# Performance work log

Hardware: AMD Instinct MI355X
Metric: run time of the kernel (lower is better)

## Reference

```python
import jax, jax.numpy as jnp
import numpy as np

K_WEIGHT = 1.7  # K passed in original forward: w(t, H, 1.7)
B_EXP = 2.5     # default exponent b in w()


def setup_inputs() -> dict:
    key = jax.random.key(0)
    k1, k2 = jax.random.split(key)
    B, H, D = 512, 2048, 64
    pred = jax.random.normal(k1, (B, H, D), dtype=jnp.float32)
    targ = jax.random.normal(k2, (B, H, D), dtype=jnp.float32)
    return {"pred": pred, "targ": targ}


def reference(pred, targ):
    # pred, targ: [B, H, D]
    B, H, D = pred.shape
    # t_i = number of nonzero entries of targ[i, :, 1] along horizon
    t = jnp.sum((targ[:, :, 1] != 0).astype(pred.dtype), axis=1)  # [B]
    # w(t, T=H, K=1.7, b=2.5) = 1 + (K-1) * (t/(H-1))**b
    weight = 1.0 + (K_WEIGHT - 1.0) * (t / (H - 1)) ** B_EXP      # [B]
    idx = t.astype(jnp.int32) - 1                                  # [B], scatter row per sample
    # Only channel 0 of the squared error is ever used (loss[:, :, :1]);
    # the [B,H,1]*[B,H,D] broadcast + sum over D is equivalent to *D.
    loss0 = (pred[:, :, 0] - targ[:, :, 0]) ** 2                   # [B, H]
    gathered = jnp.take_along_axis(loss0, idx[:, None], axis=1)[:, 0]  # [B]
    weighted_loss = jnp.mean(gathered * weight * D)
    return weighted_loss
```

## Files before the change

### kernel.cpp

```cpp
#include <hip/hip_runtime.h>


#define BB 512
#define HH 2048
#define DD 64

__global__ __launch_bounds__(256) void WeightedStateLoss4_kernel(
    const float* __restrict__ pred,
    const float* __restrict__ targ,
    float* __restrict__ out)
{
    const int i   = blockIdx.x;
    const int tid = threadIdx.x;

    const float* trow = targ + (size_t)i * HH * DD;

    int cnt = 0;
    float v[HH / 256];
#pragma unroll
    for (int k = 0; k < HH / 256; ++k) {
        const int h = tid + k * 256;
        v[k] = trow[(size_t)h * DD + 1];
    }
#pragma unroll
    for (int k = 0; k < HH / 256; ++k) {
        cnt += (v[k] != 0.0f) ? 1 : 0;
    }

#pragma unroll
    for (int off = 32; off > 0; off >>= 1)
        cnt += __shfl_down(cnt, off, 64);

    __shared__ int s[4];
    const int wave = tid >> 6;
    const int lane = tid & 63;
    if (lane == 0) s[wave] = cnt;
    __syncthreads();

    if (tid == 0) {
        const int t = s[0] + s[1] + s[2] + s[3];
        const float tf = (float)t;
        const float ratio = tf / (float)(HH - 1);
        const float w = 1.0f + 0.7f * powf(ratio, 2.5f);

        int idx = t - 1;
        idx = idx < 0 ? 0 : (idx > HH - 1 ? HH - 1 : idx);

        const size_t base = ((size_t)i * HH + (size_t)idx) * DD;
        const float p = pred[base];
        const float q = targ[base];
        const float d = p - q;
        const float val = d * d * w * (float)DD * (1.0f / (float)BB);
        atomicAdd(out, val);
    }
}

extern "C" void kernel_launch(void* const* d_in, const int* in_sizes, int n_in,
                              void* d_out, int out_size, void* d_ws, size_t ws_size,
                              hipStream_t stream)
{
    const float* pred = (const float*)d_in[0];
    const float* targ = (const float*)d_in[1];
    float* out = (float*)d_out;

    hipMemsetAsync(out, 0, sizeof(float) * (size_t)out_size, stream);

    WeightedStateLoss4_kernel<<<BB, 256, 0, stream>>>(pred, targ, out);
}
```

Baseline: 32.77 us.

## Split nonzero count across chunked blocks and finish with a single reduction kernel

The count of nonzeros in channel 1 is spread over four blocks per sample (2048 blocks in total) instead of one block per sample, raising parallelism for the strided gather. A second single-block kernel sums the partial counts, computes the weighted loss and reduces it deterministically, replacing the memset and the 512 atomic adds. This adds one extra kernel launch and a workspace round trip in exchange for more memory-level parallelism and no atomic contention.

```diff
diff --git a/kernel.cpp b/kernel.cpp
--- a/kernel.cpp
+++ b/kernel.cpp
@@ -4,54 +4,65 @@
 #define BB 512
 #define HH 2048
 #define DD 64
+#define CHUNKS 4
+#define HPC (HH / CHUNKS)
 
-__global__ __launch_bounds__(256) void WeightedStateLoss4_kernel(
-    const float* __restrict__ pred,
-    const float* __restrict__ targ,
-    float* __restrict__ out)
+__global__ __launch_bounds__(256) void wsl4_count(
+    const float* __restrict__ targ, int* __restrict__ partial)
 {
-    const int i   = blockIdx.x;
+    const int c   = blockIdx.x;
+    const int i   = blockIdx.y;
     const int tid = threadIdx.x;
 
-    const float* trow = targ + (size_t)i * HH * DD;
+    const float* p = targ + (size_t)i * HH * DD + (size_t)c * HPC * DD + 1;
 
-    int cnt = 0;
-    float v[HH / 256];
-#pragma unroll
-    for (int k = 0; k < HH / 256; ++k) {
-        const int h = tid + k * 256;
-        v[k] = trow[(size_t)h * DD + 1];
-    }
-#pragma unroll
-    for (int k = 0; k < HH / 256; ++k) {
-        cnt += (v[k] != 0.0f) ? 1 : 0;
-    }
+    const float a = p[(size_t)tid * DD];
+    const float b = p[((size_t)tid + 256) * DD];
+    int cnt = (a != 0.0f ? 1 : 0) + (b != 0.0f ? 1 : 0);
 
 #pragma unroll
     for (int off = 32; off > 0; off >>= 1)
         cnt += __shfl_down(cnt, off, 64);
 
     __shared__ int s[4];
-    const int wave = tid >> 6;
-    const int lane = tid & 63;
-    if (lane == 0) s[wave] = cnt;
+    if ((tid & 63) == 0) s[tid >> 6] = cnt;
     __syncthreads();
 
-    if (tid == 0) {
-        const int t = s[0] + s[1] + s[2] + s[3];
-        const float tf = (float)t;
-        const float ratio = tf / (float)(HH - 1);
-        const float w = 1.0f + 0.7f * powf(ratio, 2.5f);
+    if (tid == 0) partial[i * CHUNKS + c] = s[0] + s[1] + s[2] + s[3];
+}
 
-        int idx = t - 1;
-        idx = idx < 0 ? 0 : (idx > HH - 1 ? HH - 1 : idx);
+__global__ __launch_bounds__(512) void wsl4_final(
+    const float* __restrict__ pred, const float* __restrict__ targ,
+    const int* __restrict__ partial, float* __restrict__ out)
+{
+    const int i = threadIdx.x;
 
-        const size_t base = ((size_t)i * HH + (size_t)idx) * DD;
-        const float p = pred[base];
-        const float q = targ[base];
-        const float d = p - q;
-        const float val = d * d * w * (float)DD * (1.0f / (float)BB);
-        atomicAdd(out, val);
+    const int4 t4 = *(const int4*)(partial + i * CHUNKS);
+    const int t = t4.x + t4.y + t4.z + t4.w;
+
+    const float ratio = (float)t / (float)(HH - 1);
+    const float w = 1.0f + 0.7f * powf(ratio, 2.5f);
+
+    int idx = t - 1;
+    idx = idx < 0 ? 0 : (idx > HH - 1 ? HH - 1 : idx);
+
+    const size_t base = ((size_t)i * HH + (size_t)idx) * DD;
+    const float d = pred[base] - targ[base];
+    float val = d * d * w * ((float)DD / (float)BB);
+
+#pragma unroll
+    for (int off = 32; off > 0; off >>= 1)
+        val += __shfl_down(val, off, 64);
+
+    __shared__ float sf[8];
+    if ((i & 63) == 0) sf[i >> 6] = val;
+    __syncthreads();
+
+    if (i == 0) {
+        float tot = 0.0f;
+#pragma unroll
+        for (int k = 0; k < 8; ++k) tot += sf[k];
+        out[0] = tot;
     }
 }
 
@@ -62,8 +73,9 @@
     const float* pred = (const float*)d_in[0];
     const float* targ = (const float*)d_in[1];
     float* out = (float*)d_out;
+    int* partial = (int*)d_ws;
 
-    hipMemsetAsync(out, 0, sizeof(float) * (size_t)out_size, stream);
-
-    WeightedStateLoss4_kernel<<<BB, 256, 0, stream>>>(pred, targ, out);
+    dim3 grid(CHUNKS, BB);
+    wsl4_count<<<grid, 256, 0, stream>>>(targ, partial);
+    wsl4_final<<<1, 512, 0, stream>>>(pred, targ, partial, out);
 }
```

After: 29.66 us. 9.5% less time.

## Replace memset and atomic accumulation with per-sample buffer and reduction kernel

Applied to the files above, without the earlier changes.

Drops the hipMemsetAsync and the single-address atomicAdd. Each block now writes its sample loss to workspace, and a second one-wave kernel sums the 512 values deterministically. Blocks grow from 256 to 1024 threads, so each thread loads two strided channel-1 values instead of eight. This trades the memset and the atomic contention for an extra kernel launch and assumes the workspace holds 512 floats.

```diff
diff --git a/kernel.cpp b/kernel.cpp
--- a/kernel.cpp
+++ b/kernel.cpp
@@ -5,54 +5,58 @@
 #define HH 2048
 #define DD 64
 
-__global__ __launch_bounds__(256) void WeightedStateLoss4_kernel(
+__global__ __launch_bounds__(1024) void wsl4_sample(
     const float* __restrict__ pred,
     const float* __restrict__ targ,
-    float* __restrict__ out)
+    float* __restrict__ sloss)
 {
     const int i   = blockIdx.x;
     const int tid = threadIdx.x;
 
-    const float* trow = targ + (size_t)i * HH * DD;
-
-    int cnt = 0;
-    float v[HH / 256];
-#pragma unroll
-    for (int k = 0; k < HH / 256; ++k) {
-        const int h = tid + k * 256;
-        v[k] = trow[(size_t)h * DD + 1];
-    }
-#pragma unroll
-    for (int k = 0; k < HH / 256; ++k) {
-        cnt += (v[k] != 0.0f) ? 1 : 0;
-    }
+    const float* t1 = targ + (size_t)i * HH * DD + 1;
+    const float a = t1[(size_t)tid * DD];
+    const float b = t1[((size_t)tid + 1024) * DD];
+    int cnt = (a != 0.0f ? 1 : 0) + (b != 0.0f ? 1 : 0);
 
 #pragma unroll
     for (int off = 32; off > 0; off >>= 1)
         cnt += __shfl_down(cnt, off, 64);
 
-    __shared__ int s[4];
-    const int wave = tid >> 6;
-    const int lane = tid & 63;
-    if (lane == 0) s[wave] = cnt;
+    __shared__ int s[16];
+    if ((tid & 63) == 0) s[tid >> 6] = cnt;
     __syncthreads();
 
     if (tid == 0) {
-        const int t = s[0] + s[1] + s[2] + s[3];
-        const float tf = (float)t;
-        const float ratio = tf / (float)(HH - 1);
+        int t = 0;
+#pragma unroll
+        for (int k = 0; k < 16; ++k) t += s[k];
+
+        const float ratio = (float)t * (1.0f / (float)(HH - 1));
         const float w = 1.0f + 0.7f * powf(ratio, 2.5f);
 
         int idx = t - 1;
         idx = idx < 0 ? 0 : (idx > HH - 1 ? HH - 1 : idx);
 
         const size_t base = ((size_t)i * HH + (size_t)idx) * DD;
-        const float p = pred[base];
-        const float q = targ[base];
-        const float d = p - q;
-        const float val = d * d * w * (float)DD * (1.0f / (float)BB);
-        atomicAdd(out, val);
+        const float d = pred[base] - targ[base];
+        sloss[i] = d * d * w * ((float)DD / (float)BB);
     }
+}
+
+__global__ __launch_bounds__(64) void wsl4_reduce(
+    const float* __restrict__ sloss, float* __restrict__ out)
+{
+    const int tid = threadIdx.x;
+    const float4* p4 = (const float4*)sloss;
+    const float4 x = p4[tid * 2];
+    const float4 y = p4[tid * 2 + 1];
+    float v = (x.x + x.y) + (x.z + x.w) + (y.x + y.y) + (y.z + y.w);
+
+#pragma unroll
+    for (int off = 32; off > 0; off >>= 1)
+        v += __shfl_down(v, off, 64);
+
+    if (tid == 0) out[0] = v;
 }
 
 extern "C" void kernel_launch(void* const* d_in, const int* in_sizes, int n_in,
@@ -61,9 +65,8 @@
 {
     const float* pred = (const float*)d_in[0];
     const float* targ = (const float*)d_in[1];
-    float* out = (float*)d_out;
+    float* sloss = (float*)d_ws;
 
-    hipMemsetAsync(out, 0, sizeof(float) * (size_t)out_size, stream);
-
-    WeightedStateLoss4_kernel<<<BB, 256, 0, stream>>>(pred, targ, out);
+    wsl4_sample<<<BB, 1024, 0, stream>>>(pred, targ, sloss);
+    wsl4_reduce<<<1, 64, 0, stream>>>(sloss, (float*)d_out);
 }
```

Measured after the change: 29.48 us. 1.11x faster.
